# Kernel optimization log

Hardware: AMD Instinct MI355X
Metric: run time of the kernel (lower is better)

The kernel has to match this reference:

```python
import jax, jax.numpy as jnp
import numpy as np

ALPHA = 50.0
EPS = 1e-12  # torch F.normalize eps


def setup_inputs() -> dict:
    key = jax.random.key(0)
    k1, k2 = jax.random.split(key)
    N, C, H, W_sp, K = 64, 128, 64, 64, 64
    x = jax.random.normal(k1, (N, C, H, W_sp), dtype=jnp.float32)
    # centroids.permute(1,0): shape [C, K]; orthogonal-ish init approximated by scaled gaussian
    W = jax.random.normal(k2, (C, K), dtype=jnp.float32) * (1.0 / np.sqrt(C))
    bias = jnp.zeros((K,), dtype=jnp.float32)
    return {"x": x, "W": W, "bias": bias}


def _l2norm(v, axis):
    return v / jnp.maximum(jnp.linalg.norm(v, axis=axis, keepdims=True), EPS)


def reference(x, W, bias):
    N, C, H, W_sp = x.shape
    K = W.shape[1]
    x = _l2norm(x, axis=1)                      # normalize over channels
    xf = x.reshape(N, C, H * W_sp)              # [N, C, P]
    Wn = _l2norm(W, axis=0)                     # column-normalized weight [C, K]
    # soft assignment logits, computed directly in [N, K, P] layout
    sa_logits = jnp.einsum('ncp,ck->nkp', xf, Wn)
    sa = jax.nn.softmax((sa_logits + bias[None, :, None]) * ALPHA, axis=1)  # over clusters
    # VLAD via two GEMM-like contractions instead of the [N,K,C,P] residual tensor:
    # vlad[n,k,c] = sum_p sa[n,k,p] * xf[n,c,p] - W[c,k] * sum_p sa[n,k,p]
    vlad = jnp.einsum('nkp,ncp->nkc', sa, xf) - sa.sum(axis=-1)[:, :, None] * W.T[None]
    vlad = _l2norm(vlad, axis=2)                # intra-normalize per cluster
    vlad = vlad.reshape(N, K * C)
    vlad = _l2norm(vlad, axis=1)                # global L2
    return (vlad, sa_logits)                    # original returns soft_assign_ permuted to [N, K, P]
```

## Files before the change

kernel.cpp:

```cpp
#include <hip/hip_runtime.h>
#include <math.h>

#define ALPHA 50.0f
#define EPS 1e-12f

constexpr int N = 64, C = 128, P = 4096, K = 64;
constexpr int NCH2 = 16;

typedef short short8_t __attribute__((ext_vector_type(8)));
typedef short short4_t __attribute__((ext_vector_type(4)));
typedef float f4 __attribute__((ext_vector_type(4)));
typedef unsigned int u32x4 __attribute__((ext_vector_type(4)));
typedef unsigned int u32x2 __attribute__((ext_vector_type(2)));

__device__ __forceinline__ unsigned short f2bf(float f) {
    union { float f; unsigned u; } v; v.f = f;
    unsigned r = (v.u + 0x7FFFu + ((v.u >> 16) & 1u)) >> 16;
    return (unsigned short)r;
}

__device__ __forceinline__ unsigned cvtpk(float lo, float hi) {
    unsigned r;
    asm("v_cvt_pk_bf16_f32 %0, %1, %2" : "=v"(r) : "v"(lo), "v"(hi));
    return r;
}

__device__ __forceinline__ void bar_lds() {
    asm volatile("s_waitcnt lgkmcnt(0)" ::: "memory");
    __builtin_amdgcn_s_barrier();
}

__global__ __launch_bounds__(256, 3) void k_fused(
    const float* __restrict__ x, const float* __restrict__ W,
    const float* __restrict__ bias, float* __restrict__ logits,
    float* __restrict__ vlad_part, float* __restrict__ Spart,
    float* __restrict__ ss2acc)
{
    __shared__ __align__(16) char smem[51968];
    unsigned short* xsT  = (unsigned short*)smem;
    unsigned short* xsN  = (unsigned short*)(smem + 17408);
    float*          saf  = (float*)smem;
    unsigned short* sa2s = (unsigned short*)(smem + 36864);
    float*          denom= (float*)(smem + 46080);
    float*          invs = (float*)(smem + 50432);
    float*          biass= (float*)(smem + 50688);
    float*          red  = (float*)(smem + 50944);
    float*          Wl   = (float*)smem;

    const int tid  = threadIdx.x;
    const int n    = blockIdx.x >> 4;
    const int blk16= blockIdx.x & 15;
    const int pbase = blk16 * 256;

    const int w = tid >> 6, lane = tid & 63;
    const int q = lane >> 4, l15 = lane & 15;
    const int pxg = tid & 15, cg = tid >> 4;

    if (blockIdx.x == 0 && tid < 64) ss2acc[tid] = 0.f;
    if (tid < K) biass[tid] = bias[tid] * ALPHA;

    const float* xrow = x + (size_t)n * C * P + pbase + 4 * pxg;
    float4 va[8], vb[8];
    short8_t af[4];

    {
        float4 wv[8];
        #pragma unroll
        for (int it = 0; it < 8; ++it)
            wv[it] = *(const float4*)&W[(size_t)(tid + it * 256) * 4];
        #pragma unroll
        for (int j = 0; j < 8; ++j)
            va[j] = *(const float4*)&xrow[(size_t)(8 * cg + j) * P];
        #pragma unroll
        for (int it = 0; it < 8; ++it) {
            const int idx4 = tid + it * 256;
            *(float4*)&Wl[(idx4 >> 4) * 68 + (idx4 & 15) * 4] = wv[it];
        }
        bar_lds();
        {
            const int k = tid & 63, part = tid >> 6;
            float s = 0.f;
            #pragma unroll
            for (int i = 0; i < 32; ++i) {
                float v = Wl[(part * 32 + i) * 68 + k];
                s = fmaf(v, v, s);
            }
            red[tid] = s;
        }
        bar_lds();
        if (tid < 64)
            invs[tid] = 1.0f / fmaxf(
                sqrtf(red[tid] + red[64 + tid] + red[128 + tid] + red[192 + tid]), EPS);
        bar_lds();
        {
            const float cv = invs[16 * w + l15];
            #pragma unroll
            for (int c0 = 0; c0 < 4; ++c0)
                #pragma unroll
                for (int j = 0; j < 8; ++j)
                    af[c0][j] = (short)f2bf(
                        Wl[(c0 * 32 + 8 * q + j) * 68 + 16 * w + l15] * cv);
        }
    }

    f4 acc2[8];
    #pragma unroll
    for (int ct = 0; ct < 8; ++ct) acc2[ct] = (f4){0.f, 0.f, 0.f, 0.f};
    float Sreg = 0.f;

    const int pbT8 = 8 * (cg ^ (pxg & 7));
    const int l4 = l15 >> 2;

    for (int ch = 0; ch < 4; ++ch) {
        if (ch < 3) {
            const float* xb = xrow + (ch + 1) * 64;
            #pragma unroll
            for (int j = 0; j < 8; ++j)
                vb[j] = *(const float4*)&xb[(size_t)(8 * cg + j) * P];
        }
        bar_lds();
        const int p0 = pbase + ch * 64;
        const float* vf = (const float*)va;

        float pss[4] = {0.f, 0.f, 0.f, 0.f};
        #pragma unroll
        for (int j = 0; j < 8; ++j)
            #pragma unroll
            for (int i = 0; i < 4; ++i)
                pss[i] = fmaf(vf[j * 4 + i], vf[j * 4 + i], pss[i]);
        float* rd2 = denom;
        #pragma unroll
        for (int i = 0; i < 4; ++i) rd2[(4 * pxg + i) * 17 + cg] = pss[i];

        #pragma unroll
        for (int i = 0; i < 4; ++i) {
            u32x4 t;
            #pragma unroll
            for (int jj = 0; jj < 4; ++jj)
                t[jj] = cvtpk(vf[(2 * jj) * 4 + i], vf[(2 * jj + 1) * 4 + i]);
            *(u32x4*)&xsT[(4 * pxg + i) * 136 + pbT8] = t;
        }
        #pragma unroll
        for (int j = 0; j < 8; ++j) {
            u32x2 t2;
            t2[0] = cvtpk(vf[j * 4 + 0], vf[j * 4 + 1]);
            t2[1] = cvtpk(vf[j * 4 + 2], vf[j * 4 + 3]);
            *(u32x2*)&xsN[(8 * cg + j) * 76 + 4 * pxg] = t2;
        }
        bar_lds();

        if (tid < 64) {
            float s = 0.f;
            #pragma unroll
            for (int g = 0; g < 16; ++g) s += rd2[tid * 17 + g];
            invs[tid] = 1.0f / fmaxf(sqrtf(s), EPS);
        }
        f4 acc1[4];
        #pragma unroll
        for (int t = 0; t < 4; ++t) acc1[t] = (f4){0.f, 0.f, 0.f, 0.f};
        __builtin_amdgcn_s_setprio(1);
        #pragma unroll
        for (int c0 = 0; c0 < 4; ++c0)
            #pragma unroll
            for (int pxt = 0; pxt < 4; ++pxt) {
                const int pb = (4 * c0 + q) ^ (4 * (pxt & 1) + l4);
                short8_t bf = *(const short8_t*)&xsT[(pxt * 16 + l15) * 136 + pb * 8];
                acc1[pxt] = __builtin_amdgcn_mfma_f32_16x16x32_bf16(af[c0], bf, acc1[pxt], 0, 0, 0);
            }
        __builtin_amdgcn_s_setprio(0);
        bar_lds();

        float* lgp = logits + (size_t)n * K * P + p0;
        float bz[4];
        #pragma unroll
        for (int r = 0; r < 4; ++r) bz[r] = biass[16 * w + 4 * q + r];
        #pragma unroll
        for (int pxt = 0; pxt < 4; ++pxt) {
            const int pxl = pxt * 16 + l15;
            const float iv = invs[pxl];
            float psum = 0.f;
            #pragma unroll
            for (int r = 0; r < 4; ++r) {
                const int k = 16 * w + 4 * q + r;
                const float lv = acc1[pxt][r] * iv;
                __builtin_nontemporal_store(lv, &lgp[(size_t)k * P + pxl]);
                const float e = __expf(fmaf(lv, ALPHA, bz[r]));
                saf[k * 68 + pxl] = e;
                psum += e;
            }
            denom[(4 * w + q) * 68 + pxl] = psum;
        }
        bar_lds();

        {
            float dinv = 0.f;
            if (lane < 16) {
                const int pxr = 16 * w + lane;
                float dd = 0.f;
                #pragma unroll
                for (int g = 0; g < 16; ++g) dd += denom[g * 68 + pxr];
                dinv = 1.0f / dd;
            }
            const float* sp = &saf[lane * 68 + 16 * w];
            const float* ip = &invs[16 * w];
            float s = 0.f;
            unsigned pk[8];
            #pragma unroll
            for (int m = 0; m < 4; ++m) {
                f4 e  = *(const f4*)&sp[4 * m];
                f4 iv = *(const f4*)&ip[4 * m];
                const float r0 = __shfl(dinv, 4 * m + 0);
                const float r1 = __shfl(dinv, 4 * m + 1);
                const float r2 = __shfl(dinv, 4 * m + 2);
                const float r3 = __shfl(dinv, 4 * m + 3);
                s += e[0] * r0; s += e[1] * r1;
                s += e[2] * r2; s += e[3] * r3;
                const float v0 = e[0] * (r0 * iv[0]);
                const float v1 = e[1] * (r1 * iv[1]);
                const float v2 = e[2] * (r2 * iv[2]);
                const float v3 = e[3] * (r3 * iv[3]);
                pk[2 * m]     = cvtpk(v0, v1);
                pk[2 * m + 1] = cvtpk(v2, v3);
            }
            Sreg += s;
            *(u32x4*)&sa2s[lane * 72 + 16 * w]     = (u32x4){pk[0], pk[1], pk[2], pk[3]};
            *(u32x4*)&sa2s[lane * 72 + 16 * w + 8] = (u32x4){pk[4], pk[5], pk[6], pk[7]};
        }
        bar_lds();

        short8_t a2[2];
        #pragma unroll
        for (int kit = 0; kit < 2; ++kit)
            a2[kit] = *(const short8_t*)&sa2s[(16 * w + l15) * 72 + kit * 32 + 8 * q];
        __builtin_amdgcn_s_setprio(1);
        #pragma unroll
        for (int ct = 0; ct < 8; ++ct)
            #pragma unroll
            for (int kit = 0; kit < 2; ++kit) {
                const unsigned short* bp = &xsN[(ct * 16 + l15) * 76 + kit * 32 + 8 * q];
                short4_t b0 = *(const short4_t*)bp;
                short4_t b1 = *(const short4_t*)(bp + 4);
                short8_t bb;
                bb[0] = b0[0]; bb[1] = b0[1]; bb[2] = b0[2]; bb[3] = b0[3];
                bb[4] = b1[0]; bb[5] = b1[1]; bb[6] = b1[2]; bb[7] = b1[3];
                acc2[ct] = __builtin_amdgcn_mfma_f32_16x16x32_bf16(a2[kit], bb, acc2[ct], 0, 0, 0);
            }
        __builtin_amdgcn_s_setprio(0);

        if (ch < 3) {
            #pragma unroll
            for (int j = 0; j < 8; ++j) va[j] = vb[j];
        }
    }

    float* vp = vlad_part + ((size_t)blk16 * N + n) * (size_t)(K * C);
    #pragma unroll
    for (int ct = 0; ct < 8; ++ct)
        #pragma unroll
        for (int r = 0; r < 4; ++r)
            vp[(16 * w + 4 * q + r) * C + ct * 16 + l15] = acc2[ct][r];

    red[tid] = Sreg;
    __syncthreads();
    if (tid < 64)
        Spart[((size_t)blk16 * N + n) * K + tid] =
            red[tid] + red[64 + tid] + red[128 + tid] + red[192 + tid];
}

__global__ __launch_bounds__(256) void k_post1(
    const float* __restrict__ vlad_part, const float* __restrict__ W,
    const float* __restrict__ Spart, float* __restrict__ out,
    float* __restrict__ ss2acc)
{
    __shared__ float red[16];
    const int tid = threadIdx.x;
    const int n  = blockIdx.x >> 2;
    const int kq = blockIdx.x & 3;
    const int kl = tid >> 4;
    const int ci = tid & 15;
    const int k  = kq * 16 + kl;
    const int c0 = ci * 8;

    float Sk = 0.f;
    #pragma unroll
    for (int ch = 0; ch < NCH2; ++ch) Sk += Spart[(size_t)(ch * N + n) * K + k];

    float v[8];
    #pragma unroll
    for (int l = 0; l < 8; ++l) v[l] = 0.f;
    #pragma unroll
    for (int ch = 0; ch < NCH2; ++ch) {
        const float* vp = vlad_part + ((size_t)(ch * N + n) * K + k) * C + c0;
        float4 a = *(const float4*)&vp[0];
        float4 b = *(const float4*)&vp[4];
        v[0] += a.x; v[1] += a.y; v[2] += a.z; v[3] += a.w;
        v[4] += b.x; v[5] += b.y; v[6] += b.z; v[7] += b.w;
    }

    float ss = 0.f;
    #pragma unroll
    for (int l = 0; l < 8; ++l) {
        float val = v[l] - W[(size_t)(c0 + l) * K + k] * Sk;
        v[l] = val;
        ss = fmaf(val, val, ss);
    }
    ss += __shfl_xor(ss, 1);
    ss += __shfl_xor(ss, 2);
    ss += __shfl_xor(ss, 4);
    ss += __shfl_xor(ss, 8);
    const float inv1 = 1.0f / fmaxf(sqrtf(ss), EPS);
    float ss2 = 0.f;
    #pragma unroll
    for (int l = 0; l < 8; ++l) { v[l] *= inv1; ss2 = fmaf(v[l], v[l], ss2); }
    ss2 += __shfl_xor(ss2, 1);
    ss2 += __shfl_xor(ss2, 2);
    ss2 += __shfl_xor(ss2, 4);
    ss2 += __shfl_xor(ss2, 8);
    if (ci == 0) red[kl] = ss2;
    __syncthreads();
    if (tid == 0) {
        float t = 0.f;
        #pragma unroll
        for (int i = 0; i < 16; ++i) t += red[i];
        atomicAdd(&ss2acc[n], t);
    }

    float* op = out + (size_t)n * K * C + (size_t)k * C + c0;
    *(float4*)&op[0] = (float4){v[0], v[1], v[2], v[3]};
    *(float4*)&op[4] = (float4){v[4], v[5], v[6], v[7]};
}

__global__ __launch_bounds__(256) void k_post2(
    float* __restrict__ out, const float* __restrict__ ss2acc)
{
    const int n   = blockIdx.x >> 2;
    const int seg = blockIdx.x & 3;
    const float inv2 = 1.0f / fmaxf(sqrtf(ss2acc[n]), EPS);
    float* p = out + (size_t)n * K * C + (size_t)seg * 2048 + (size_t)threadIdx.x * 8;
    float4 a = *(const float4*)&p[0];
    float4 b = *(const float4*)&p[4];
    a.x *= inv2; a.y *= inv2; a.z *= inv2; a.w *= inv2;
    b.x *= inv2; b.y *= inv2; b.z *= inv2; b.w *= inv2;
    *(float4*)&p[0] = a;
    *(float4*)&p[4] = b;
}

extern "C" void kernel_launch(void* const* d_in, const int* in_sizes, int n_in,
                              void* d_out, int out_size, void* d_ws, size_t ws_size,
                              hipStream_t stream)
{
    const float* x    = (const float*)d_in[0];
    const float* W    = (const float*)d_in[1];
    const float* bias = (const float*)d_in[2];

    float* out_vlad   = (float*)d_out;
    float* out_logits = (float*)d_out + (size_t)N * K * C;

    float* ss2acc     = (float*)((char*)d_ws + 16384);
    float* Spart      = (float*)((char*)d_ws + 32768);
    float* vlad_part  = (float*)((char*)d_ws + 32768 + 262144);

    k_fused<<<dim3(N * NCH2), dim3(256), 0, stream>>>(
        x, W, bias, out_logits, vlad_part, Spart, ss2acc);
    k_post1<<<dim3(N * 4), dim3(256), 0, stream>>>(vlad_part, W, Spart, out_vlad, ss2acc);
    k_post2<<<dim3(N * 4), dim3(256), 0, stream>>>(out_vlad, ss2acc);
}
```

Baseline: 276.2 us.

## Halve fused-kernel grid and software-pipeline the VLAD GEMM with double-buffered xsN

Each block now covers 512 pixels in 8 chunks instead of 256 in 4, so the grid is halved and fewer partial VLAD results go to the workspace. The second MFMA contraction for chunk i is deferred into iteration i+1 and reads a double-buffered xsN tile, so it overlaps with converting and staging the next chunk. LDS grows to about 71 KB and the launch bound drops to 2 blocks per CU, trading occupancy for a grid that fits in a single wave and for more overlap.

```diff
diff --git a/kernel.cpp b/kernel.cpp
--- a/kernel.cpp
+++ b/kernel.cpp
@@ -5,7 +5,7 @@
 #define EPS 1e-12f
 
 constexpr int N = 64, C = 128, P = 4096, K = 64;
-constexpr int NCH2 = 16;
+constexpr int NCH2 = 8;
 
 typedef short short8_t __attribute__((ext_vector_type(8)));
 typedef short short4_t __attribute__((ext_vector_type(4)));
@@ -30,27 +30,26 @@
     __builtin_amdgcn_s_barrier();
 }
 
-__global__ __launch_bounds__(256, 3) void k_fused(
+__global__ __launch_bounds__(256, 2) void k_fused(
     const float* __restrict__ x, const float* __restrict__ W,
     const float* __restrict__ bias, float* __restrict__ logits,
     float* __restrict__ vlad_part, float* __restrict__ Spart,
     float* __restrict__ ss2acc)
 {
-    __shared__ __align__(16) char smem[51968];
+    __shared__ __align__(16) char smem[71424];
     unsigned short* xsT  = (unsigned short*)smem;
-    unsigned short* xsN  = (unsigned short*)(smem + 17408);
     float*          saf  = (float*)smem;
-    unsigned short* sa2s = (unsigned short*)(smem + 36864);
-    float*          denom= (float*)(smem + 46080);
-    float*          invs = (float*)(smem + 50432);
-    float*          biass= (float*)(smem + 50688);
-    float*          red  = (float*)(smem + 50944);
+    unsigned short* sa2s = (unsigned short*)(smem + 56320);
+    float*          denom= (float*)(smem + 65536);
+    float*          invs = (float*)(smem + 69888);
+    float*          biass= (float*)(smem + 70144);
+    float*          red  = (float*)(smem + 70400);
     float*          Wl   = (float*)smem;
 
     const int tid  = threadIdx.x;
-    const int n    = blockIdx.x >> 4;
-    const int blk16= blockIdx.x & 15;
-    const int pbase = blk16 * 256;
+    const int n    = blockIdx.x >> 3;
+    const int blk8 = blockIdx.x & 7;
+    const int pbase = blk8 * 512;
 
     const int w = tid >> 6, lane = tid & 63;
     const int q = lane >> 4, l15 = lane & 15;
@@ -101,6 +100,7 @@
                     af[c0][j] = (short)f2bf(
                         Wl[(c0 * 32 + 8 * q + j) * 68 + 16 * w + l15] * cv);
         }
+        bar_lds();
     }
 
     f4 acc2[8];
@@ -111,45 +111,68 @@
     const int pbT8 = 8 * (cg ^ (pxg & 7));
     const int l4 = l15 >> 2;
 
-    for (int ch = 0; ch < 4; ++ch) {
-        if (ch < 3) {
+    for (int ch = 0; ch < 8; ++ch) {
+        if (ch < 7) {
             const float* xb = xrow + (ch + 1) * 64;
             #pragma unroll
             for (int j = 0; j < 8; ++j)
                 vb[j] = *(const float4*)&xb[(size_t)(8 * cg + j) * P];
         }
-        bar_lds();
-        const int p0 = pbase + ch * 64;
-        const float* vf = (const float*)va;
-
-        float pss[4] = {0.f, 0.f, 0.f, 0.f};
-        #pragma unroll
-        for (int j = 0; j < 8; ++j)
-            #pragma unroll
-            for (int i = 0; i < 4; ++i)
-                pss[i] = fmaf(vf[j * 4 + i], vf[j * 4 + i], pss[i]);
-        float* rd2 = denom;
-        #pragma unroll
-        for (int i = 0; i < 4; ++i) rd2[(4 * pxg + i) * 17 + cg] = pss[i];
-
-        #pragma unroll
-        for (int i = 0; i < 4; ++i) {
-            u32x4 t;
-            #pragma unroll
-            for (int jj = 0; jj < 4; ++jj)
-                t[jj] = cvtpk(vf[(2 * jj) * 4 + i], vf[(2 * jj + 1) * 4 + i]);
-            *(u32x4*)&xsT[(4 * pxg + i) * 136 + pbT8] = t;
-        }
-        #pragma unroll
-        for (int j = 0; j < 8; ++j) {
-            u32x2 t2;
-            t2[0] = cvtpk(vf[j * 4 + 0], vf[j * 4 + 1]);
-            t2[1] = cvtpk(vf[j * 4 + 2], vf[j * 4 + 3]);
-            *(u32x2*)&xsN[(8 * cg + j) * 76 + 4 * pxg] = t2;
+        if (ch > 0) {
+            const unsigned short* xsNr =
+                (const unsigned short*)(smem + 17408 + 19456 * ((ch - 1) & 1));
+            short8_t a2[2];
+            #pragma unroll
+            for (int kit = 0; kit < 2; ++kit)
+                a2[kit] = *(const short8_t*)&sa2s[(16 * w + l15) * 72 + kit * 32 + 8 * q];
+            __builtin_amdgcn_s_setprio(1);
+            #pragma unroll
+            for (int ct = 0; ct < 8; ++ct)
+                #pragma unroll
+                for (int kit = 0; kit < 2; ++kit) {
+                    const unsigned short* bp = &xsNr[(ct * 16 + l15) * 76 + kit * 32 + 8 * q];
+                    short4_t b0 = *(const short4_t*)bp;
+                    short4_t b1 = *(const short4_t*)(bp + 4);
+                    short8_t bb;
+                    bb[0] = b0[0]; bb[1] = b0[1]; bb[2] = b0[2]; bb[3] = b0[3];
+                    bb[4] = b1[0]; bb[5] = b1[1]; bb[6] = b1[2]; bb[7] = b1[3];
+                    acc2[ct] = __builtin_amdgcn_mfma_f32_16x16x32_bf16(a2[kit], bb, acc2[ct], 0, 0, 0);
+                }
+            __builtin_amdgcn_s_setprio(0);
+        }
+        {
+            unsigned short* xsNw = (unsigned short*)(smem + 17408 + 19456 * (ch & 1));
+            const float* vf = (const float*)va;
+            float pss[4] = {0.f, 0.f, 0.f, 0.f};
+            #pragma unroll
+            for (int j = 0; j < 8; ++j)
+                #pragma unroll
+                for (int i = 0; i < 4; ++i)
+                    pss[i] = fmaf(vf[j * 4 + i], vf[j * 4 + i], pss[i]);
+            float* rd2 = denom;
+            #pragma unroll
+            for (int i = 0; i < 4; ++i) rd2[(4 * pxg + i) * 17 + cg] = pss[i];
+
+            #pragma unroll
+            for (int i = 0; i < 4; ++i) {
+                u32x4 t;
+                #pragma unroll
+                for (int jj = 0; jj < 4; ++jj)
+                    t[jj] = cvtpk(vf[(2 * jj) * 4 + i], vf[(2 * jj + 1) * 4 + i]);
+                *(u32x4*)&xsT[(4 * pxg + i) * 136 + pbT8] = t;
+            }
+            #pragma unroll
+            for (int j = 0; j < 8; ++j) {
+                u32x2 t2;
+                t2[0] = cvtpk(vf[j * 4 + 0], vf[j * 4 + 1]);
+                t2[1] = cvtpk(vf[j * 4 + 2], vf[j * 4 + 3]);
+                *(u32x2*)&xsNw[(8 * cg + j) * 76 + 4 * pxg] = t2;
+            }
         }
         bar_lds();
 
         if (tid < 64) {
+            const float* rd2 = denom;
             float s = 0.f;
             #pragma unroll
             for (int g = 0; g < 16; ++g) s += rd2[tid * 17 + g];
@@ -170,25 +193,28 @@
         __builtin_amdgcn_s_setprio(0);
         bar_lds();
 
-        float* lgp = logits + (size_t)n * K * P + p0;
-        float bz[4];
-        #pragma unroll
-        for (int r = 0; r < 4; ++r) bz[r] = biass[16 * w + 4 * q + r];
-        #pragma unroll
-        for (int pxt = 0; pxt < 4; ++pxt) {
-            const int pxl = pxt * 16 + l15;
-            const float iv = invs[pxl];
-            float psum = 0.f;
-            #pragma unroll
-            for (int r = 0; r < 4; ++r) {
-                const int k = 16 * w + 4 * q + r;
-                const float lv = acc1[pxt][r] * iv;
-                __builtin_nontemporal_store(lv, &lgp[(size_t)k * P + pxl]);
-                const float e = __expf(fmaf(lv, ALPHA, bz[r]));
-                saf[k * 68 + pxl] = e;
-                psum += e;
-            }
-            denom[(4 * w + q) * 68 + pxl] = psum;
+        {
+            const int p0 = pbase + ch * 64;
+            float* lgp = logits + (size_t)n * K * P + p0;
+            float bz[4];
+            #pragma unroll
+            for (int r = 0; r < 4; ++r) bz[r] = biass[16 * w + 4 * q + r];
+            #pragma unroll
+            for (int pxt = 0; pxt < 4; ++pxt) {
+                const int pxl = pxt * 16 + l15;
+                const float iv = invs[pxl];
+                float psum = 0.f;
+                #pragma unroll
+                for (int r = 0; r < 4; ++r) {
+                    const int k = 16 * w + 4 * q + r;
+                    const float lv = acc1[pxt][r] * iv;
+                    __builtin_nontemporal_store(lv, &lgp[(size_t)k * P + pxl]);
+                    const float e = __expf(fmaf(lv, ALPHA, bz[r]));
+                    saf[k * 68 + pxl] = e;
+                    psum += e;
+                }
+                denom[(4 * w + q) * 68 + pxl] = psum;
+            }
         }
         bar_lds();
 
@@ -228,6 +254,14 @@
         }
         bar_lds();
 
+        if (ch < 7) {
+            #pragma unroll
+            for (int j = 0; j < 8; ++j) va[j] = vb[j];
+        }
+    }
+
+    {
+        const unsigned short* xsNr = (const unsigned short*)(smem + 17408 + 19456 * 1);
         short8_t a2[2];
         #pragma unroll
         for (int kit = 0; kit < 2; ++kit)
@@ -237,7 +271,7 @@
         for (int ct = 0; ct < 8; ++ct)
             #pragma unroll
             for (int kit = 0; kit < 2; ++kit) {
-                const unsigned short* bp = &xsN[(ct * 16 + l15) * 76 + kit * 32 + 8 * q];
+                const unsigned short* bp = &xsNr[(ct * 16 + l15) * 76 + kit * 32 + 8 * q];
                 short4_t b0 = *(const short4_t*)bp;
                 short4_t b1 = *(const short4_t*)(bp + 4);
                 short8_t bb;
@@ -246,14 +280,9 @@
                 acc2[ct] = __builtin_amdgcn_mfma_f32_16x16x32_bf16(a2[kit], bb, acc2[ct], 0, 0, 0);
             }
         __builtin_amdgcn_s_setprio(0);
-
-        if (ch < 3) {
-            #pragma unroll
-            for (int j = 0; j < 8; ++j) va[j] = vb[j];
-        }
-    }
-
-    float* vp = vlad_part + ((size_t)blk16 * N + n) * (size_t)(K * C);
+    }
+
+    float* vp = vlad_part + ((size_t)blk8 * N + n) * (size_t)(K * C);
     #pragma unroll
     for (int ct = 0; ct < 8; ++ct)
         #pragma unroll
@@ -263,7 +292,7 @@
     red[tid] = Sreg;
     __syncthreads();
     if (tid < 64)
-        Spart[((size_t)blk16 * N + n) * K + tid] =
+        Spart[((size_t)blk8 * N + n) * K + tid] =
             red[tid] + red[64 + tid] + red[128 + tid] + red[192 + tid];
 }
 
@@ -358,7 +387,7 @@
 
     float* ss2acc     = (float*)((char*)d_ws + 16384);
     float* Spart      = (float*)((char*)d_ws + 32768);
-    float* vlad_part  = (float*)((char*)d_ws + 32768 + 262144);
+    float* vlad_part  = (float*)((char*)d_ws + 32768 + 131072);
 
     k_fused<<<dim3(N * NCH2), dim3(256), 0, stream>>>(
         x, W, bias, out_logits, vlad_part, Spart, ss2acc);
```

After: 235.9 us. 14.6% less time.
